# Kernel optimization log

Hardware: AMD Instinct MI355X
Metric: run time of the kernel (lower is better)

The kernel has to match this reference:

```python
import jax, jax.numpy as jnp
import numpy as np

B, T, D = 2, 2048, 1024
H = 16
HD = D // H


def setup_inputs() -> dict:
    key = jax.random.key(0)
    ks = jax.random.split(key, 9)
    s = 1.0 / np.sqrt(D)
    return {
        "x": jax.random.normal(ks[0], (B, T, D), dtype=jnp.float32),
        "Wq": jax.random.normal(ks[1], (D, D), dtype=jnp.float32) * s,
        "bq": jax.random.normal(ks[2], (D,), dtype=jnp.float32) * s,
        "Wk": jax.random.normal(ks[3], (D, D), dtype=jnp.float32) * s,
        "bk": jax.random.normal(ks[4], (D,), dtype=jnp.float32) * s,
        "Wv": jax.random.normal(ks[5], (D, D), dtype=jnp.float32) * s,
        "bv": jax.random.normal(ks[6], (D,), dtype=jnp.float32) * s,
        "Wo": jax.random.normal(ks[7], (D, D), dtype=jnp.float32) * s,
        "bo": jax.random.normal(ks[8], (D,), dtype=jnp.float32) * s,
    }


def reference(x, Wq, bq, Wk, bk, Wv, bv, Wo, bo):
    b, t, d = x.shape
    # projections; torch Linear computes x @ W.T + b
    def proj(W, bias):
        y = jnp.einsum("btd,ed->bte", x, W) + bias
        return y.reshape(b, t, H, HD).transpose(0, 2, 1, 3)  # [B,H,T,HD]
    q = proj(Wq, bq)
    k = proj(Wk, bk)
    v = proj(Wv, bv)
    scores = jnp.einsum("bhqd,bhkd->bhqk", q, k) / np.sqrt(HD)  # [B,H,T,T]
    causal = jnp.triu(jnp.ones((t, t), dtype=bool), k=1)
    scores = jnp.where(causal[None, None], jnp.float32(-1e9), scores)
    attn = jax.nn.softmax(scores, axis=-1)
    out = jnp.einsum("bhqk,bhkd->bhqd", attn, v)  # [B,H,T,HD]
    out = out.transpose(0, 2, 1, 3).reshape(b, t, d)
    return jnp.einsum("btd,ed->bte", out, Wo) + bo
```

## Files before the change

### kernel.cpp

```cpp
#include <hip/hip_runtime.h>


#define DEV __device__ __forceinline__

typedef __attribute__((ext_vector_type(8))) __bf16 bf16x8;
typedef __attribute__((ext_vector_type(4))) float f32x4;

DEV unsigned short f2bf(float f) {
  union { float f; unsigned u; } c;
  c.f = f;
  unsigned u = c.u + 0x7FFFu + ((c.u >> 16) & 1u);
  return (unsigned short)(u >> 16);
}

DEV unsigned cvtpk(float lo, float hi) {
  unsigned r;
  asm("v_cvt_pk_bf16_f32 %0, %1, %2" : "=v"(r) : "v"(lo), "v"(hi));
  return r;
}

DEV void gload16(const unsigned short* g, unsigned short* l) {
  __builtin_amdgcn_global_load_lds(
      (const __attribute__((address_space(1))) unsigned int*)g,
      (__attribute__((address_space(3))) unsigned int*)l, 16, 0, 0);
}

DEV f32x4 mfma16(bf16x8 a, bf16x8 b, f32x4 c) {
  return __builtin_amdgcn_mfma_f32_16x16x32_bf16(a, b, c, 0, 0, 0);
}

#define WAITVM(n) asm volatile("s_waitcnt vmcnt(" #n ")" ::: "memory")
#define WAITLGKM() asm volatile("s_waitcnt lgkmcnt(0)" ::: "memory")
#define BAR() __builtin_amdgcn_s_barrier()
#define SCHEDB() __builtin_amdgcn_sched_barrier(0)
#define PRIO(n) __builtin_amdgcn_s_setprio(n)

__global__ __launch_bounds__(256) void k_cvt_all(
    const float* __restrict__ x, const float* __restrict__ wq,
    const float* __restrict__ wk, const float* __restrict__ wv,
    const float* __restrict__ wo, unsigned short* __restrict__ dst) {
  int i = blockIdx.x * blockDim.x + threadIdx.x;
  const float* s;
  int off;
  if (i < 1048576) {
    s = x; off = i;
  } else {
    int j = i - 1048576;
    int w = j >> 18;
    off = j & 262143;
    s = (w == 0) ? wq : (w == 1) ? wk : (w == 2) ? wv : wo;
  }
  float4 v = reinterpret_cast<const float4*>(s)[off];
  uint2 o;
  o.x = (unsigned)f2bf(v.x) | ((unsigned)f2bf(v.y) << 16);
  o.y = (unsigned)f2bf(v.z) | ((unsigned)f2bf(v.w) << 16);
  reinterpret_cast<uint2*>(dst)[i] = o;
}

__global__ __launch_bounds__(256) void k_gemm_qkv(
    const unsigned short* __restrict__ X, const unsigned short* __restrict__ Wq,
    const unsigned short* __restrict__ Wk, const unsigned short* __restrict__ Wv,
    const float* __restrict__ bq, const float* __restrict__ bk,
    const float* __restrict__ bv, unsigned short* __restrict__ Qo,
    unsigned short* __restrict__ Ko, unsigned short* __restrict__ Vo) {
  __shared__ unsigned short ls[20480];
  unsigned short* la0 = ls;
  unsigned short* lbq = ls + 8192;
  unsigned short* lbk = ls + 12288;
  unsigned short* lbv = ls + 16384;

  const int id = blockIdx.x;
  const int xcd = id & 7, s4 = id >> 3;
  const int bx = ((s4 >> 3) & 7) * 2 + (xcd & 1);
  const int by = (s4 & 7) * 4 + (xcd >> 1);
  const int m0 = by * 128, n0 = bx * 64;

  const int tid = threadIdx.x;
  const int lane = tid & 63, wave = tid >> 6;
  const int l15 = lane & 15, g = lane >> 4;
  const int wm = (wave >> 1) * 64, wn = (wave & 1) * 32;
  const int g16 = g << 4;
  const int sx = (lane & 3) << 4;

  f32x4 a0[4][2] = {}, a1[4][2] = {}, a2[4][2] = {};

#define STG_QKV(buf, k0)                                                     \
  {                                                                          \
    _Pragma("unroll") for (int i = 0; i < 2; ++i) {                          \
      const int c = i * 256 + tid;                                           \
      const int row = c >> 2;                                                \
      const int scb = ((c & 3) << 4) ^ ((row & 3) << 4);                     \
      gload16(X + (m0 + row) * 1024 + (k0) + (scb >> 1),                     \
              (unsigned short*)((char*)(la0 + (buf)*4096) + c * 16));        \
    }                                                                        \
    {                                                                        \
      const int row = tid >> 2;                                              \
      const int scb = ((tid & 3) << 4) ^ ((row & 3) << 4);                   \
      const int go = (n0 + row) * 1024 + (k0) + (scb >> 1);                  \
      gload16(Wq + go,                                                       \
              (unsigned short*)((char*)(lbq + (buf)*2048) + tid * 16));      \
      gload16(Wk + go,                                                       \
              (unsigned short*)((char*)(lbk + (buf)*2048) + tid * 16));      \
      gload16(Wv + go,                                                       \
              (unsigned short*)((char*)(lbv + (buf)*2048) + tid * 16));      \
    }                                                                        \
  }

  STG_QKV(0, 0);
  __syncthreads();

  for (int kt = 0; kt < 32; ++kt) {
    const int cur = kt & 1;
    if (kt + 1 < 32) STG_QKV(cur ^ 1, (kt + 1) * 32);
    unsigned short* la = la0 + cur * 4096;
    bf16x8 af[4];
#pragma unroll
    for (int m = 0; m < 4; ++m)
      af[m] = *reinterpret_cast<const bf16x8*>(
          (char*)la + (wm + m * 16 + l15) * 64 + (g16 ^ sx));
    {
      unsigned short* lb = lbq + cur * 2048;
      bf16x8 bfr[2];
#pragma unroll
      for (int n = 0; n < 2; ++n)
        bfr[n] = *reinterpret_cast<const bf16x8*>(
            (char*)lb + (wn + n * 16 + l15) * 64 + (g16 ^ sx));
#pragma unroll
      for (int m = 0; m < 4; ++m)
#pragma unroll
        for (int n = 0; n < 2; ++n) a0[m][n] = mfma16(af[m], bfr[n], a0[m][n]);
    }
    {
      unsigned short* lb = lbk + cur * 2048;
      bf16x8 bfr[2];
#pragma unroll
      for (int n = 0; n < 2; ++n)
        bfr[n] = *reinterpret_cast<const bf16x8*>(
            (char*)lb + (wn + n * 16 + l15) * 64 + (g16 ^ sx));
#pragma unroll
      for (int m = 0; m < 4; ++m)
#pragma unroll
        for (int n = 0; n < 2; ++n) a1[m][n] = mfma16(af[m], bfr[n], a1[m][n]);
    }
    {
      unsigned short* lb = lbv + cur * 2048;
      bf16x8 bfr[2];
#pragma unroll
      for (int n = 0; n < 2; ++n)
        bfr[n] = *reinterpret_cast<const bf16x8*>(
            (char*)lb + (wn + n * 16 + l15) * 64 + (g16 ^ sx));
#pragma unroll
      for (int m = 0; m < 4; ++m)
#pragma unroll
        for (int n = 0; n < 2; ++n) a2[m][n] = mfma16(af[m], bfr[n], a2[m][n]);
    }
    __syncthreads();
  }
#undef STG_QKV

  unsigned short* lw = ls + wave * 2048;
  const int h = (n0 + wn) >> 6;
  const int hd0 = (n0 + wn) & 63;
  const int rb = m0 + wm;
  const int b = rb >> 11;
  const int tb0 = rb & 2047;

#pragma unroll
  for (int mode = 0; mode < 2; ++mode) {
    const float* bias = mode ? bk : bq;
    const float sc = mode ? 1.0f : 0.180336880f;
    unsigned short* dst = mode ? Ko : Qo;
    WAITLGKM();
#pragma unroll
    for (int m = 0; m < 4; ++m)
#pragma unroll
      for (int n = 0; n < 2; ++n) {
        const float bb = bias[n0 + wn + n * 16 + l15];
        const f32x4 av = mode ? a1[m][n] : a0[m][n];
#pragma unroll
        for (int r = 0; r < 4; ++r)
          lw[(m * 16 + (g << 2) + r) * 32 + n * 16 + l15] =
              f2bf((av[r] + bb) * sc);
      }
    WAITLGKM();
    SCHEDB();
#pragma unroll
    for (int it = 0; it < 4; ++it) {
      const int rr = (lane >> 2) + it * 16;
      const int ck = (lane & 3) * 8;
      uint4 v = *reinterpret_cast<const uint4*>(&lw[rr * 32 + ck]);
      *reinterpret_cast<uint4*>(
          &dst[(((b << 4) + h) * 2048 + tb0 + rr) * 64 + hd0 + ck]) = v;
    }
  }

  WAITLGKM();
#pragma unroll
  for (int m = 0; m < 4; ++m)
#pragma unroll
    for (int n = 0; n < 2; ++n) {
      const float bb = bv[n0 + wn + n * 16 + l15];
      uint2 w;
      w.x = cvtpk(a2[m][n][0] + bb, a2[m][n][1] + bb);
      w.y = cvtpk(a2[m][n][2] + bb, a2[m][n][3] + bb);
      *reinterpret_cast<uint2*>(&lw[(n * 16 + l15) * 64 + m * 16 + (g << 2)]) =
          w;
    }
  WAITLGKM();
  SCHEDB();
#pragma unroll
  for (int it = 0; it < 4; ++it) {
    const int hdr = (lane >> 3) + it * 8;
    const int ck = (lane & 7) * 8;
    uint4 v = *reinterpret_cast<const uint4*>(&lw[hdr * 64 + ck]);
    *reinterpret_cast<uint4*>(
        &Vo[(((b << 4) + h) * 64 + hd0 + hdr) * 2048 + tb0 + ck]) = v;
  }
}

__global__ __launch_bounds__(256) void k_gemm_out(
    const unsigned short* __restrict__ Ctx, const unsigned short* __restrict__ Wo,
    const float* __restrict__ bo, float* __restrict__ Out) {
  __shared__ unsigned short ls[16384];
  unsigned short* la0 = ls;
  unsigned short* lb0 = ls + 8192;
  const int id = blockIdx.x;
  const int xcd = id & 7, s4 = id >> 3;
  const int bx = ((s4 >> 3) & 7) * 2 + (xcd & 1);
  const int by = (s4 & 7) * 4 + (xcd >> 1);
  const int tid = threadIdx.x;
  const int lane = tid & 63, wave = tid >> 6;
  const int l15 = lane & 15, g = lane >> 4;
  const int m0 = by * 128, n0 = bx * 64;
  const int wm = (wave >> 1) * 64, wn = (wave & 1) * 32;
  const int g16 = (g << 4);
  const int sx = (lane & 3) << 4;
  f32x4 acc[4][2] = {};

#define STG_OUT(buf, k0)                                                     \
  {                                                                          \
    _Pragma("unroll") for (int i = 0; i < 2; ++i) {                          \
      const int c = i * 256 + tid;                                           \
      const int row = c >> 2;                                                \
      const int scb = (((c & 3) << 4)) ^ ((row & 3) << 4);                   \
      gload16(Ctx + (m0 + row) * 1024 + (k0) + (scb >> 1),                   \
              (unsigned short*)((char*)(la0 + (buf)*4096) + c * 16));        \
    }                                                                        \
    {                                                                        \
      const int row = tid >> 2;                                              \
      const int scb = (((tid & 3) << 4)) ^ ((row & 3) << 4);                 \
      gload16(Wo + (n0 + row) * 1024 + (k0) + (scb >> 1),                    \
              (unsigned short*)((char*)(lb0 + (buf)*2048) + tid * 16));      \
    }                                                                        \
  }

  STG_OUT(0, 0);
  __syncthreads();

  for (int kt = 0; kt < 32; ++kt) {
    const int cur = kt & 1;
    unsigned short* la = la0 + cur * 4096;
    unsigned short* lb = lb0 + cur * 2048;
    if (kt + 1 < 32) STG_OUT(cur ^ 1, (kt + 1) * 32);
    bf16x8 af[4], bfr[2];
#pragma unroll
    for (int m = 0; m < 4; ++m)
      af[m] = *reinterpret_cast<const bf16x8*>(
          (char*)la + (wm + m * 16 + l15) * 64 + (g16 ^ sx));
#pragma unroll
    for (int n = 0; n < 2; ++n)
      bfr[n] = *reinterpret_cast<const bf16x8*>(
          (char*)lb + (wn + n * 16 + l15) * 64 + (g16 ^ sx));
#pragma unroll
    for (int m = 0; m < 4; ++m)
#pragma unroll
      for (int n = 0; n < 2; ++n)
        acc[m][n] = mfma16(af[m], bfr[n], acc[m][n]);
    __syncthreads();
  }
#undef STG_OUT

  float* lwf = (float*)(ls + wave * 4096);
#pragma unroll
  for (int m = 0; m < 4; ++m)
#pragma unroll
    for (int n = 0; n < 2; ++n) {
      const float bb = bo[n0 + wn + n * 16 + l15];
#pragma unroll
      for (int r = 0; r < 4; ++r)
        lwf[(m * 16 + (g << 2) + r) * 32 + n * 16 + l15] = acc[m][n][r] + bb;
    }
  WAITLGKM();
  SCHEDB();
#pragma unroll
  for (int it = 0; it < 8; ++it) {
    const int rr = (lane >> 3) + it * 8;
    const int ck = (lane & 7) * 4;
    float4 v = *reinterpret_cast<const float4*>(&lwf[rr * 32 + ck]);
    *reinterpret_cast<float4*>(&Out[(m0 + wm + rr) * 1024 + n0 + wn + ck]) = v;
  }
}


DEV void attn_stage128(const unsigned short* __restrict__ Kb,
                       const unsigned short* __restrict__ Vb,
                       unsigned short* lk, unsigned short* lv, int kv0,
                       int tid) {
#pragma unroll
  for (int i = 0; i < 2; ++i) {
    const int c = i * 512 + tid;
    const int krow = c >> 3;
    const int kscb = ((c & 7) << 4) ^ ((krow & 7) << 4);
    gload16(Kb + (kv0 + krow) * 64 + (kscb >> 1),
            (unsigned short*)((char*)lk + c * 16));
    const int vrow = c >> 4;
    const int vscb = ((c & 15) << 4) ^ ((vrow & 7) << 4);
    gload16(Vb + vrow * 2048 + kv0 + (vscb >> 1),
            (unsigned short*)((char*)lv + c * 16));
  }
}

DEV void attn_step(const unsigned short* lk128, int s,
                   const unsigned short* lv128,
                   unsigned short (&lp)[16][64], const bf16x8 (&qf)[2],
                   f32x4 (&o)[4], float& lsum, int lane, int qloc, bool diag) {
  const int g = lane >> 4;
  const int l15 = lane & 15;
  f32x4 st[4];
  PRIO(1);
#pragma unroll
  for (int n = 0; n < 4; ++n) {
    f32x4 z = {};
    const int row = n * 16 + l15;
    const int sw = (row & 7) << 4;
#pragma unroll
    for (int kk = 0; kk < 2; ++kk) {
      bf16x8 kf = *reinterpret_cast<const bf16x8*>(
          (char*)lk128 + (s * 64 + row) * 128 + ((kk * 64 + (g << 4)) ^ sw));
      z = mfma16(kf, qf[kk], z);
    }
    st[n] = z;
  }
  PRIO(0);
  if (diag) {
#pragma unroll
    for (int n = 0; n < 4; ++n)
#pragma unroll
      for (int r = 0; r < 4; ++r)
        if (n * 16 + g * 4 + r > qloc) st[n][r] = -1e30f;
  }
  float rs = 0.f;
#pragma unroll
  for (int n = 0; n < 4; ++n)
#pragma unroll
    for (int r = 0; r < 4; ++r) {
      float p = exp2f(st[n][r]);
      st[n][r] = p;
      rs += p;
    }
  lsum += rs;
  const int psw = (l15 & 7) << 4;
#pragma unroll
  for (int n = 0; n < 4; ++n) {
    uint2 w;
    w.x = cvtpk(st[n][0], st[n][1]);
    w.y = cvtpk(st[n][2], st[n][3]);
    *reinterpret_cast<uint2*>(
        (char*)lp + l15 * 128 + (((n << 5) | (g << 3)) ^ psw)) = w;
  }
  WAITLGKM();
  SCHEDB();
  bf16x8 pb[2];
  pb[0] = *reinterpret_cast<const bf16x8*>(
      (char*)lp + l15 * 128 + (((g << 4)) ^ psw));
  pb[1] = *reinterpret_cast<const bf16x8*>(
      (char*)lp + l15 * 128 + ((64 + (g << 4)) ^ psw));
  PRIO(1);
#pragma unroll
  for (int h = 0; h < 4; ++h) {
    const int vr = h * 16 + l15;
    const int sw = (vr & 7) << 4;
#pragma unroll
    for (int kk = 0; kk < 2; ++kk) {
      bf16x8 vf = *reinterpret_cast<const bf16x8*>(
          (char*)lv128 + vr * 256 + ((s * 128 + kk * 64 + (g << 4)) ^ sw));
      o[h] = mfma16(vf, pb[kk], o[h]);
    }
  }
  PRIO(0);
}

DEV void attn_epi(unsigned short* __restrict__ Ctx,
                  unsigned short (&lp)[16][64], const f32x4 (&o)[4],
                  float lsum, int b, int hh, int qbase, int lane) {
  float lt = lsum;
  lt += __shfl_xor(lt, 16);
  lt += __shfl_xor(lt, 32);
  const float inv = 1.f / lt;
  const int g = lane >> 4;
  const int l15 = lane & 15;
  const int psw = (l15 & 7) << 4;
#pragma unroll
  for (int h = 0; h < 4; ++h) {
    uint2 w;
    w.x = cvtpk(o[h][0] * inv, o[h][1] * inv);
    w.y = cvtpk(o[h][2] * inv, o[h][3] * inv);
    *reinterpret_cast<uint2*>(
        (char*)lp + l15 * 128 + (((h << 5) | (g << 3)) ^ psw)) = w;
  }
  WAITLGKM();
  SCHEDB();
#pragma unroll
  for (int it = 0; it < 2; ++it) {
    const int q = (lane >> 3) + it * 8;
    const int blk = (lane & 7) ^ (q & 7);
    uint4 v = *reinterpret_cast<const uint4*>((char*)lp + q * 128 + blk * 16);
    *reinterpret_cast<uint4*>(
        &Ctx[(b * 2048 + qbase + q) * 1024 + hh * 64 + ((lane & 7) << 3)]) = v;
  }
}

__global__ __launch_bounds__(512) void k_attn(
    const unsigned short* __restrict__ Q, const unsigned short* __restrict__ K,
    const unsigned short* __restrict__ Vt, unsigned short* __restrict__ Ctx) {
  __shared__ unsigned short lk[2][8192];
  __shared__ unsigned short lv[2][8192];
  __shared__ unsigned short lp[8][16][64];

  const int tid = threadIdx.x, lane = tid & 63, wave = tid >> 6;
  const int id = blockIdx.x;
  const int xcd = id & 7, r4 = id >> 3;
  const int ip = r4 & 15;
  const int bh = ((r4 >> 4) << 3) + xcd;

  const int qtA = ip;
  const int qtB = 31 - ip;
  const int nb = (qtB >> 1) + 1;

  const bool isB = wave < 4;
  const int wv4 = wave & 3;
  const int qt = isB ? qtB : qtA;

  const unsigned short* Kb = K + bh * 2048 * 64;
  const unsigned short* Vb = Vt + bh * 64 * 2048;

  bf16x8 qf[2];
  {
    const unsigned short* qr =
        Q + (bh * 2048 + qt * 64 + wv4 * 16 + (lane & 15)) * 64 +
        ((lane >> 4) << 3);
    qf[0] = *reinterpret_cast<const bf16x8*>(qr);
    qf[1] = *reinterpret_cast<const bf16x8*>(qr + 32);
  }

  f32x4 o[4] = {};
  float lsum = 0.f;
  const int qloc = wv4 * 16 + (lane & 15);

  attn_stage128(Kb, Vb, lk[0], lv[0], 0, tid);

  for (int t = 0; t < nb; ++t) {
    WAITVM(0);
    BAR();
    {
      const int nx = (t + 1 < nb) ? t + 1 : nb - 1;
      attn_stage128(Kb, Vb, lk[(t + 1) & 1], lv[(t + 1) & 1], nx * 128, tid);
    }
    SCHEDB();
    const unsigned short* lkc = lk[t & 1];
    const unsigned short* lvc = lv[t & 1];
#pragma unroll
    for (int s = 0; s < 2; ++s) {
      const int sub = 2 * t + s;
      if (sub <= qt)
        attn_step(lkc, s, lvc, lp[wave], qf, o, lsum, lane, qloc, sub == qt);
    }
  }

  WAITVM(0);

  const int b = bh >> 4, hh = bh & 15;
  attn_epi(Ctx, lp[wave], o, lsum, b, hh, qt * 64 + wv4 * 16, lane);
}

extern "C" void kernel_launch(void* const* d_in, const int* in_sizes, int n_in,
                              void* d_out, int out_size, void* d_ws,
                              size_t ws_size, hipStream_t stream) {
  const float* x = (const float*)d_in[0];
  const float* Wq = (const float*)d_in[1];
  const float* bq = (const float*)d_in[2];
  const float* Wk = (const float*)d_in[3];
  const float* bk = (const float*)d_in[4];
  const float* Wv = (const float*)d_in[5];
  const float* bv = (const float*)d_in[6];
  const float* Wo = (const float*)d_in[7];
  const float* bo = (const float*)d_in[8];
  float* out = (float*)d_out;

  char* ws = (char*)d_ws;
  unsigned short* xb = (unsigned short*)(ws);
  unsigned short* wqb = (unsigned short*)(ws + (8u << 20));
  unsigned short* wkb = (unsigned short*)(ws + (10u << 20));
  unsigned short* wvb = (unsigned short*)(ws + (12u << 20));
  unsigned short* wob = (unsigned short*)(ws + (14u << 20));
  unsigned short* Qb = (unsigned short*)(ws + (16u << 20));
  unsigned short* Kb = (unsigned short*)(ws + (24u << 20));
  unsigned short* Vtb = (unsigned short*)(ws + (32u << 20));
  unsigned short* Ctx = (unsigned short*)(ws + (40u << 20));

  k_cvt_all<<<8192, 256, 0, stream>>>(x, Wq, Wk, Wv, Wo, xb);

  k_gemm_qkv<<<512, 256, 0, stream>>>(xb, wqb, wkb, wvb, bq, bk, bv,
                                      Qb, Kb, Vtb);
  k_attn<<<512, 512, 0, stream>>>(Qb, Kb, Vtb, Ctx);
  k_gemm_out<<<512, 256, 0, stream>>>(Ctx, wob, bo, out);
}
```

Measured before the change: 106.8 us.

## Switch attention to 32x32 MFMA with register-resident P and triple-buffered KV

Rewrites the attention kernel to use 32x32x16 bf16 MFMA with 32 query rows per wave. The P matrix is passed into the PV product through v_permlane32_swap instead of a round trip through LDS. The kernel now uses 4 waves per block, a 64-wide KV tile and three LDS buffers, so two stages stay in flight. This is meant to cut LDS traffic and per-MFMA overhead, at the cost of more accumulator registers per wave and fewer waves per block.

```diff
diff --git a/kernel.cpp b/kernel.cpp
--- a/kernel.cpp
+++ b/kernel.cpp
@@ -5,6 +5,7 @@
 
 typedef __attribute__((ext_vector_type(8))) __bf16 bf16x8;
 typedef __attribute__((ext_vector_type(4))) float f32x4;
+typedef __attribute__((ext_vector_type(16))) float f32x16;
 
 DEV unsigned short f2bf(float f) {
   union { float f; unsigned u; } c;
@@ -27,6 +28,10 @@
 
 DEV f32x4 mfma16(bf16x8 a, bf16x8 b, f32x4 c) {
   return __builtin_amdgcn_mfma_f32_16x16x32_bf16(a, b, c, 0, 0, 0);
+}
+
+DEV f32x16 mfma32(bf16x8 a, bf16x8 b, f32x16 c) {
+  return __builtin_amdgcn_mfma_f32_32x32x16_bf16(a, b, c, 0, 0, 0);
 }
 
 #define WAITVM(n) asm volatile("s_waitcnt vmcnt(" #n ")" ::: "memory")
@@ -302,130 +307,87 @@
 }
 
 
-DEV void attn_stage128(const unsigned short* __restrict__ Kb,
-                       const unsigned short* __restrict__ Vb,
-                       unsigned short* lk, unsigned short* lv, int kv0,
-                       int tid) {
+DEV void attn_stage64(const unsigned short* __restrict__ Kb,
+                      const unsigned short* __restrict__ Vb,
+                      unsigned short* lk, unsigned short* lv, int kv0,
+                      int tid) {
 #pragma unroll
   for (int i = 0; i < 2; ++i) {
-    const int c = i * 512 + tid;
-    const int krow = c >> 3;
-    const int kscb = ((c & 7) << 4) ^ ((krow & 7) << 4);
-    gload16(Kb + (kv0 + krow) * 64 + (kscb >> 1),
-            (unsigned short*)((char*)lk + c * 16));
-    const int vrow = c >> 4;
-    const int vscb = ((c & 15) << 4) ^ ((vrow & 7) << 4);
-    gload16(Vb + vrow * 2048 + kv0 + (vscb >> 1),
-            (unsigned short*)((char*)lv + c * 16));
-  }
-}
-
-DEV void attn_step(const unsigned short* lk128, int s,
-                   const unsigned short* lv128,
-                   unsigned short (&lp)[16][64], const bf16x8 (&qf)[2],
-                   f32x4 (&o)[4], float& lsum, int lane, int qloc, bool diag) {
-  const int g = lane >> 4;
-  const int l15 = lane & 15;
-  f32x4 st[4];
+    const int c = i * 256 + tid;
+    const int row = c >> 3;
+    const int scb = ((c & 7) << 4) ^ ((row & 7) << 4);
+    gload16(Kb + (kv0 + row) * 64 + (scb >> 1), lk + c * 8);
+    gload16(Vb + row * 2048 + kv0 + (scb >> 1), lv + c * 8);
+  }
+}
+
+DEV void attn_step32(const unsigned short* lk, const unsigned short* lv,
+                     const bf16x8 (&qf)[4], f32x16& O0, f32x16& O1,
+                     float& ls, int lane, int sub, int kvg0, int qg,
+                     bool diag) {
+  const int l31 = lane & 31;
+  const int hi = lane >> 5;
+  const int h16 = hi << 4;
+  const int sw = (l31 & 7) << 4;
+  f32x16 st = {};
   PRIO(1);
 #pragma unroll
-  for (int n = 0; n < 4; ++n) {
-    f32x4 z = {};
-    const int row = n * 16 + l15;
-    const int sw = (row & 7) << 4;
-#pragma unroll
-    for (int kk = 0; kk < 2; ++kk) {
-      bf16x8 kf = *reinterpret_cast<const bf16x8*>(
-          (char*)lk128 + (s * 64 + row) * 128 + ((kk * 64 + (g << 4)) ^ sw));
-      z = mfma16(kf, qf[kk], z);
-    }
-    st[n] = z;
+  for (int m = 0; m < 4; ++m) {
+    bf16x8 kf = *reinterpret_cast<const bf16x8*>(
+        (const char*)lk + (sub * 32 + l31) * 128 + ((m * 32 + h16) ^ sw));
+    st = mfma32(kf, qf[m], st);
   }
   PRIO(0);
   if (diag) {
 #pragma unroll
-    for (int n = 0; n < 4; ++n)
-#pragma unroll
-      for (int r = 0; r < 4; ++r)
-        if (n * 16 + g * 4 + r > qloc) st[n][r] = -1e30f;
+    for (int r = 0; r < 16; ++r) {
+      const int kvl = (r & 3) + 8 * (r >> 2) + 4 * hi;
+      if (kvg0 + sub * 32 + kvl > qg) st[r] = -1e30f;
+    }
   }
   float rs = 0.f;
 #pragma unroll
-  for (int n = 0; n < 4; ++n)
-#pragma unroll
-    for (int r = 0; r < 4; ++r) {
-      float p = exp2f(st[n][r]);
-      st[n][r] = p;
-      rs += p;
-    }
-  lsum += rs;
-  const int psw = (l15 & 7) << 4;
-#pragma unroll
-  for (int n = 0; n < 4; ++n) {
-    uint2 w;
-    w.x = cvtpk(st[n][0], st[n][1]);
-    w.y = cvtpk(st[n][2], st[n][3]);
-    *reinterpret_cast<uint2*>(
-        (char*)lp + l15 * 128 + (((n << 5) | (g << 3)) ^ psw)) = w;
-  }
-  WAITLGKM();
-  SCHEDB();
-  bf16x8 pb[2];
-  pb[0] = *reinterpret_cast<const bf16x8*>(
-      (char*)lp + l15 * 128 + (((g << 4)) ^ psw));
-  pb[1] = *reinterpret_cast<const bf16x8*>(
-      (char*)lp + l15 * 128 + ((64 + (g << 4)) ^ psw));
-  PRIO(1);
-#pragma unroll
-  for (int h = 0; h < 4; ++h) {
-    const int vr = h * 16 + l15;
-    const int sw = (vr & 7) << 4;
-#pragma unroll
-    for (int kk = 0; kk < 2; ++kk) {
-      bf16x8 vf = *reinterpret_cast<const bf16x8*>(
-          (char*)lv128 + vr * 256 + ((s * 128 + kk * 64 + (g << 4)) ^ sw));
-      o[h] = mfma16(vf, pb[kk], o[h]);
-    }
-  }
-  PRIO(0);
-}
-
-DEV void attn_epi(unsigned short* __restrict__ Ctx,
-                  unsigned short (&lp)[16][64], const f32x4 (&o)[4],
-                  float lsum, int b, int hh, int qbase, int lane) {
-  float lt = lsum;
-  lt += __shfl_xor(lt, 16);
-  lt += __shfl_xor(lt, 32);
-  const float inv = 1.f / lt;
-  const int g = lane >> 4;
-  const int l15 = lane & 15;
-  const int psw = (l15 & 7) << 4;
-#pragma unroll
-  for (int h = 0; h < 4; ++h) {
-    uint2 w;
-    w.x = cvtpk(o[h][0] * inv, o[h][1] * inv);
-    w.y = cvtpk(o[h][2] * inv, o[h][3] * inv);
-    *reinterpret_cast<uint2*>(
-        (char*)lp + l15 * 128 + (((h << 5) | (g << 3)) ^ psw)) = w;
-  }
-  WAITLGKM();
-  SCHEDB();
-#pragma unroll
-  for (int it = 0; it < 2; ++it) {
-    const int q = (lane >> 3) + it * 8;
-    const int blk = (lane & 7) ^ (q & 7);
-    uint4 v = *reinterpret_cast<const uint4*>((char*)lp + q * 128 + blk * 16);
-    *reinterpret_cast<uint4*>(
-        &Ctx[(b * 2048 + qbase + q) * 1024 + hh * 64 + ((lane & 7) << 3)]) = v;
-  }
-}
-
-__global__ __launch_bounds__(512) void k_attn(
+  for (int r = 0; r < 16; ++r) {
+    float p = exp2f(st[r]);
+    st[r] = p;
+    rs += p;
+  }
+  ls += rs;
+#pragma unroll
+  for (int m2 = 0; m2 < 2; ++m2) {
+    unsigned a0 = cvtpk(st[m2 * 8 + 0], st[m2 * 8 + 1]);
+    unsigned a1 = cvtpk(st[m2 * 8 + 2], st[m2 * 8 + 3]);
+    unsigned a2 = cvtpk(st[m2 * 8 + 4], st[m2 * 8 + 5]);
+    unsigned a3 = cvtpk(st[m2 * 8 + 6], st[m2 * 8 + 7]);
+    unsigned b0 = a0, b1 = a1, b2 = a2, b3 = a3;
+    asm("v_permlane32_swap_b32 %0, %1" : "+v"(a0), "+v"(b0));
+    asm("v_permlane32_swap_b32 %0, %1" : "+v"(a1), "+v"(b1));
+    asm("v_permlane32_swap_b32 %0, %1" : "+v"(a2), "+v"(b2));
+    asm("v_permlane32_swap_b32 %0, %1" : "+v"(a3), "+v"(b3));
+    union { unsigned u[4]; bf16x8 v; } pb;
+    pb.u[0] = hi ? a2 : a0;
+    pb.u[1] = hi ? a3 : a1;
+    pb.u[2] = hi ? b2 : b0;
+    pb.u[3] = hi ? b3 : b1;
+    PRIO(1);
+    {
+      const int vb = (sub * 64 + m2 * 32 + h16) ^ sw;
+      bf16x8 vf0 = *reinterpret_cast<const bf16x8*>(
+          (const char*)lv + l31 * 128 + vb);
+      O0 = mfma32(vf0, pb.v, O0);
+      bf16x8 vf1 = *reinterpret_cast<const bf16x8*>(
+          (const char*)lv + (32 + l31) * 128 + vb);
+      O1 = mfma32(vf1, pb.v, O1);
+    }
+    PRIO(0);
+  }
+}
+
+__global__ __launch_bounds__(256) void k_attn(
     const unsigned short* __restrict__ Q, const unsigned short* __restrict__ K,
     const unsigned short* __restrict__ Vt, unsigned short* __restrict__ Ctx) {
-  __shared__ unsigned short lk[2][8192];
-  __shared__ unsigned short lv[2][8192];
-  __shared__ unsigned short lp[8][16][64];
+  __shared__ unsigned short lk[3][4096];
+  __shared__ unsigned short lv[3][4096];
 
   const int tid = threadIdx.x, lane = tid & 63, wave = tid >> 6;
   const int id = blockIdx.x;
@@ -435,52 +397,82 @@
 
   const int qtA = ip;
   const int qtB = 31 - ip;
-  const int nb = (qtB >> 1) + 1;
-
-  const bool isB = wave < 4;
-  const int wv4 = wave & 3;
-  const int qt = isB ? qtB : qtA;
+  const int nt = qtB + 1;
+
+  const int qt = (wave < 2) ? qtB : qtA;
+  const int qoff = (wave & 1) << 5;
+  const int l31 = lane & 31, hi = lane >> 5;
+  const int qg = qt * 64 + qoff + l31;
 
   const unsigned short* Kb = K + bh * 2048 * 64;
   const unsigned short* Vb = Vt + bh * 64 * 2048;
 
-  bf16x8 qf[2];
+  bf16x8 qf[4];
   {
-    const unsigned short* qr =
-        Q + (bh * 2048 + qt * 64 + wv4 * 16 + (lane & 15)) * 64 +
-        ((lane >> 4) << 3);
-    qf[0] = *reinterpret_cast<const bf16x8*>(qr);
-    qf[1] = *reinterpret_cast<const bf16x8*>(qr + 32);
-  }
-
-  f32x4 o[4] = {};
-  float lsum = 0.f;
-  const int qloc = wv4 * 16 + (lane & 15);
-
-  attn_stage128(Kb, Vb, lk[0], lv[0], 0, tid);
-
-  for (int t = 0; t < nb; ++t) {
-    WAITVM(0);
+    const unsigned short* qr = Q + (bh * 2048 + qg) * 64 + (hi << 3);
+#pragma unroll
+    for (int m = 0; m < 4; ++m)
+      qf[m] = *reinterpret_cast<const bf16x8*>(qr + m * 16);
+  }
+
+  f32x16 O0 = {}, O1 = {};
+  float ls = 0.f;
+
+  attn_stage64(Kb, Vb, lk[0], lv[0], 0, tid);
+  attn_stage64(Kb, Vb, lk[1], lv[1], 64, tid);
+
+  for (int t = 0; t < nt; ++t) {
+    WAITVM(4);
     BAR();
     {
-      const int nx = (t + 1 < nb) ? t + 1 : nb - 1;
-      attn_stage128(Kb, Vb, lk[(t + 1) & 1], lv[(t + 1) & 1], nx * 128, tid);
+      const int nx = (t + 2 < nt) ? t + 2 : nt - 1;
+      attn_stage64(Kb, Vb, lk[(t + 2) % 3], lv[(t + 2) % 3], nx * 64, tid);
     }
     SCHEDB();
-    const unsigned short* lkc = lk[t & 1];
-    const unsigned short* lvc = lv[t & 1];
-#pragma unroll
-    for (int s = 0; s < 2; ++s) {
-      const int sub = 2 * t + s;
-      if (sub <= qt)
-        attn_step(lkc, s, lvc, lp[wave], qf, o, lsum, lane, qloc, sub == qt);
+    if (t <= qt) {
+      const unsigned short* lkc = lk[t % 3];
+      const unsigned short* lvc = lv[t % 3];
+      const bool dg = (t == qt);
+      attn_step32(lkc, lvc, qf, O0, O1, ls, lane, 0, t * 64, qg, dg);
+      attn_step32(lkc, lvc, qf, O0, O1, ls, lane, 1, t * 64, qg, dg);
     }
   }
 
   WAITVM(0);
-
+  BAR();
+
+  float lt = ls + __shfl_xor(ls, 32);
+  const float inv = 1.f / lt;
+  char* lw = (char*)lk + wave * 4608;
+
+#pragma unroll
+  for (int r2 = 0; r2 < 4; ++r2) {
+    const int d0 = 8 * r2 + 4 * hi;
+    uint2 w;
+    w.x = cvtpk(O0[4 * r2] * inv, O0[4 * r2 + 1] * inv);
+    w.y = cvtpk(O0[4 * r2 + 2] * inv, O0[4 * r2 + 3] * inv);
+    *reinterpret_cast<uint2*>(lw + l31 * 144 + d0 * 2) = w;
+  }
+#pragma unroll
+  for (int r2 = 0; r2 < 4; ++r2) {
+    const int d0 = 32 + 8 * r2 + 4 * hi;
+    uint2 w;
+    w.x = cvtpk(O1[4 * r2] * inv, O1[4 * r2 + 1] * inv);
+    w.y = cvtpk(O1[4 * r2 + 2] * inv, O1[4 * r2 + 3] * inv);
+    *reinterpret_cast<uint2*>(lw + l31 * 144 + d0 * 2) = w;
+  }
+  WAITLGKM();
+  SCHEDB();
+
+  const int row = lane >> 1, half = lane & 1;
+  const int qg2 = qt * 64 + qoff + row;
   const int b = bh >> 4, hh = bh & 15;
-  attn_epi(Ctx, lp[wave], o, lsum, b, hh, qt * 64 + wv4 * 16, lane);
+#pragma unroll
+  for (int k = 0; k < 4; ++k) {
+    uint4 v = *reinterpret_cast<const uint4*>(lw + row * 144 + half * 64 + k * 16);
+    *reinterpret_cast<uint4*>(
+        &Ctx[(b * 2048 + qg2) * 1024 + hh * 64 + half * 32 + k * 8]) = v;
+  }
 }
 
 extern "C" void kernel_launch(void* const* d_in, const int* in_sizes, int n_in,
@@ -512,6 +504,6 @@
 
   k_gemm_qkv<<<512, 256, 0, stream>>>(xb, wqb, wkb, wvb, bq, bk, bv,
                                       Qb, Kb, Vtb);
-  k_attn<<<512, 512, 0, stream>>>(Qb, Kb, Vtb, Ctx);
+  k_attn<<<512, 256, 0, stream>>>(Qb, Kb, Vtb, Ctx);
   k_gemm_out<<<512, 256, 0, stream>>>(Ctx, wob, bo, out);
 }
```

New measurement: 141.2 us. +32.2%, slower.
